# Kernel tuning notes

Hardware: AMD Instinct MI355X
Metric: run time of the kernel (lower is better)

## Reference

```python
import jax, jax.numpy as jnp
from jax import lax
import numpy as np

B, T, F, H, L = 256, 512, 16, 256, 2


def _lstm_layer(x, w_ih, w_hh, b_ih, b_hh):
    # x: [B, T, in]; w_ih: [4H, in]; w_hh: [4H, H]; biases: [4H]
    # PyTorch gate order: i, f, g, o
    x_proj = jnp.einsum('bti,gi->btg', x, w_ih) + b_ih + b_hh  # [B, T, 4H]
    h0 = jnp.zeros((x.shape[0], w_hh.shape[1]), x.dtype)
    c0 = h0

    def step(carry, xp):
        h, c = carry
        gates = xp + h @ w_hh.T  # [B, 4H]
        i, f, g, o = jnp.split(gates, 4, axis=-1)
        c = jax.nn.sigmoid(f) * c + jax.nn.sigmoid(i) * jnp.tanh(g)
        h = jax.nn.sigmoid(o) * jnp.tanh(c)
        return (h, c), h

    _, hs = lax.scan(step, (h0, c0), jnp.swapaxes(x_proj, 0, 1))  # [T, B, H]
    return jnp.swapaxes(hs, 0, 1)  # [B, T, H]


def setup_inputs() -> dict:
    key = jax.random.key(0)
    ks = jax.random.split(key, 16)
    x = jax.random.normal(ks[0], (B, T, F), dtype=jnp.float32)
    lengths = jax.random.randint(ks[1], (B,), 1, T + 1)  # in [1, T]
    s = 1.0 / np.sqrt(H)
    u = lambda k, shape: jax.random.uniform(k, shape, jnp.float32, -s, s)
    inp = {'x': x, 'lengths': lengths}
    in_dims = [F, H]
    for l in range(L):
        inp[f'w_ih{l}'] = u(ks[2 + 4 * l], (4 * H, in_dims[l]))
        inp[f'w_hh{l}'] = u(ks[3 + 4 * l], (4 * H, H))
        inp[f'b_ih{l}'] = u(ks[4 + 4 * l], (4 * H,))
        inp[f'b_hh{l}'] = u(ks[5 + 4 * l], (4 * H,))
    inp['fc_w'] = u(ks[10], (1, H))
    inp['fc_b'] = u(ks[11], (1,))
    return inp


def reference(x, lengths, w_ih0, w_hh0, b_ih0, b_hh0,
              w_ih1, w_hh1, b_ih1, b_hh1, fc_w, fc_b):
    # Packed LSTM: outputs at t >= length never influence last_outputs
    # (recurrence only flows forward in time), so running the dense
    # full-length LSTM and gathering at lengths-1 is mathematically identical.
    h = _lstm_layer(x, w_ih0, w_hh0, b_ih0, b_hh0)
    h = _lstm_layer(h, w_ih1, w_hh1, b_ih1, b_hh1)
    last = h[jnp.arange(h.shape[0]), lengths - 1]  # [B, H]
    return jax.nn.relu(last) @ fc_w.T + fc_b  # [B, 1]
```

## Files before the change

### kernel.cpp

```cpp
#include <hip/hip_runtime.h>
#include <hip/hip_fp16.h>


#define Tc 32
#define NCHUNK 16

#define OFF_IH0   0
#define OFF_B0    16384
#define OFF_B1    17408
#define OFF_C0S   18432
#define OFF_C1S   84480
#define OFF_H1S   150528
#define OFF_HLAST 216576
#define FP_END    282624
#define H_HH0  0
#define H_HH1  262144
#define H_IH1  524288
#define H_H0C  786432
#define H0SLOT 2113536
#define H_XP1  5013504
#define XPSLOT 8454144

#define SMEM_BYTES 149120
#define L0_WRES_OFF 50816
#define L1_WRES_OFF 17408

typedef _Float16 v2h __attribute__((ext_vector_type(2)));

__device__ __forceinline__ unsigned packh2(float a, float b) {
  __half2 h = __floats2half2_rn(a, b);
  return *(unsigned*)&h;
}
__device__ __forceinline__ float4 dot4(const float4 w, const v2h h, float4 acc) {
  const v2h* wg = (const v2h*)&w;
  acc.x = __builtin_amdgcn_fdot2(wg[0], h, acc.x, false);
  acc.y = __builtin_amdgcn_fdot2(wg[1], h, acc.y, false);
  acc.z = __builtin_amdgcn_fdot2(wg[2], h, acc.z, false);
  acc.w = __builtin_amdgcn_fdot2(wg[3], h, acc.w, false);
  return acc;
}
__device__ __forceinline__ float sigf(float x) {
  return __fdividef(1.f, 1.f + __expf(-x));
}
__device__ __forceinline__ float tanhf_fast(float x) {
  float ax = fabsf(x);
  float e = __expf(-2.f * ax);
  float t = __fdividef(1.f - e, 1.f + e);
  return copysignf(t, x);
}
__device__ __forceinline__ float h2f(unsigned short s) {
  __half h = __builtin_bit_cast(__half, s);
  return __half2float(h);
}
__device__ __forceinline__ float4 cvt4(ushort4 v) {
  float4 r;
  r.x = h2f(v.x); r.y = h2f(v.y); r.z = h2f(v.z); r.w = h2f(v.w);
  return r;
}
__device__ __forceinline__ v2h u2h(unsigned v) {
  return __builtin_bit_cast(v2h, v);
}
__device__ __forceinline__ void lds_barrier() {
  asm volatile("s_waitcnt lgkmcnt(0)" ::: "memory");
  __builtin_amdgcn_s_barrier();
  __builtin_amdgcn_sched_barrier(0);
}

__global__ __launch_bounds__(256) void prep_kernel(
    const float* __restrict__ w_ih0, const float* __restrict__ w_hh0,
    const float* __restrict__ b_ih0, const float* __restrict__ b_hh0,
    const float* __restrict__ w_ih1, const float* __restrict__ w_hh1,
    const float* __restrict__ b_ih1, const float* __restrict__ b_hh1,
    float* __restrict__ ws) {
  const int idx = blockIdx.x * blockDim.x + threadIdx.x;
  const int g = idx & 3, u = (idx >> 2) & 255, p = idx >> 10;
  const int j = g * 256 + u;
  unsigned* h16u = (unsigned*)(ws + FP_END);
  h16u[H_HH0 / 2 + idx] = packh2(w_hh0[j * 256 + 2 * p], w_hh0[j * 256 + 2 * p + 1]);
  h16u[H_HH1 / 2 + idx] = packh2(w_hh1[j * 256 + 2 * p], w_hh1[j * 256 + 2 * p + 1]);
  h16u[H_IH1 / 2 + idx] = packh2(w_ih1[j * 256 + 2 * p], w_ih1[j * 256 + 2 * p + 1]);
  if (idx < 8192) {
    ((unsigned*)(ws + OFF_IH0))[idx] =
        packh2(w_ih0[j * 16 + 2 * p], w_ih0[j * 16 + 2 * p + 1]);
  }
  if (idx < 1024) {
    ws[OFF_B0 + idx] = b_ih0[j] + b_hh0[j];
    ws[OFF_B1 + idx] = b_ih1[j] + b_hh1[j];
  }
}

__global__ __launch_bounds__(512)
__attribute__((amdgpu_waves_per_eu(2, 2)))
void fused_kernel(
    float* __restrict__ ws, const float* __restrict__ x,
    const int* __restrict__ lengths, int step) {
  extern __shared__ __align__(16) char smem_raw[];
  const int bid = blockIdx.x;
  const int tid = threadIdx.x;
  __half* h16 = (__half*)(ws + FP_END);
  unsigned short* h0cS = (unsigned short*)(h16 + H_H0C);
  unsigned short* xpS = (unsigned short*)(h16 + H_XP1);

  if (bid < 86) {
    if (step >= NCHUNK) return;
    const int kc = step;
    const int kh = tid >> 8, u = tid & 255;
    const int bg = bid * 3;
    unsigned short* hb = (unsigned short*)smem_raw;
    unsigned* xsp = (unsigned*)(smem_raw + 4096);
    float* scratch = (float*)(smem_raw + 4352);
    float4* wxl = (float4*)(smem_raw + 18048);
    float4* wres = (float4*)(smem_raw + L0_WRES_OFF);

    int len[3];
    #pragma unroll
    for (int b = 0; b < 3; ++b) len[b] = (bg + b < 256) ? lengths[bg + b] : 1;
    const int tmaxb = max(len[0], max(len[1], len[2]));
    if (kc * Tc >= tmaxb) return;
    const int tend = min(Tc, tmaxb - kc * Tc);
    const int slot = kc & 1, slotP = slot ^ 1;

    {
      const float4* gwx = (const float4*)(ws + OFF_IH0);
      #pragma unroll
      for (int e = 0; e < 4; ++e) wxl[tid + e * 512] = gwx[tid + e * 512];
    }
    {
      const float4* wgl = (const float4*)(h16 + H_HH0);
      #pragma unroll
      for (int e = 0; e < 12; ++e) {
        int i = tid + e * 512;
        int khh = (i >= 3072) ? 1 : 0;
        int r = i - khh * 3072;
        wres[i] = wgl[khh * 16384 + r];
      }
    }

    const float4* wq = (const float4*)(h16 + H_HH0) + (size_t)(kh * 64) * 256 + u;
    const float4* wrp = wres + kh * 3072 + u;
    const float4 bias = ((const float4*)(ws + OFF_B0))[u];

    float c[3] = {0.f, 0.f, 0.f};
    if (kh == 0) {
      #pragma unroll
      for (int b = 0; b < 3; ++b) {
        unsigned short hv = 0;
        if (kc > 0) {
          hv = h0cS[(size_t)slotP * H0SLOT + ((size_t)(bg + b) * 32 + 31) * 256 + u];
          c[b] = ws[OFF_C0S + (bg + b) * 256 + u];
        }
        hb[0 * 768 + b * 256 + u] = hv;
      }
    }
    if (tid < 24) {
      int b = tid >> 3, i = tid & 7;
      int bb = min(bg + b, 255);
      const float* xp = x + (size_t)bb * 8192 + (kc * Tc) * 16;
      xsp[0 * 24 + b * 8 + i] = packh2(xp[2 * i], xp[2 * i + 1]);
    }
    __syncthreads();

    float4 R[4][4];
    for (int tc = 0; tc < tend; ++tc) {
      const int cur = tc & 1, nxt = cur ^ 1;
      #pragma unroll
      for (int jp = 0; jp < 3; ++jp) {
        R[jp][0] = wq[((jp + 3) * 4 + 0) * 256];
        R[jp][1] = wq[((jp + 3) * 4 + 1) * 256];
        R[jp][2] = wq[((jp + 3) * 4 + 2) * 256];
        R[jp][3] = wq[((jp + 3) * 4 + 3) * 256];
      }
      float4 A0, A1, A2;
      if (kh == 0) { A0 = bias; A1 = bias; A2 = bias; }
      else { A0 = make_float4(0, 0, 0, 0); A1 = A0; A2 = A0; }

      #pragma unroll
      for (int p = 0; p < 4; ++p) {
        float4 w = wxl[(kh * 4 + p) * 256 + u];
        v2h x0 = u2h(xsp[cur * 24 + 0 * 8 + kh * 4 + p]);
        v2h x1 = u2h(xsp[cur * 24 + 1 * 8 + kh * 4 + p]);
        v2h x2 = u2h(xsp[cur * 24 + 2 * 8 + kh * 4 + p]);
        A0 = dot4(w, x0, A0);
        A1 = dot4(w, x1, A1);
        A2 = dot4(w, x2, A2);
      }

      const float4* h0r0 = (const float4*)(hb + cur * 768 + 0 * 256 + kh * 128);
      const float4* h0r1 = (const float4*)(hb + cur * 768 + 1 * 256 + kh * 128);
      const float4* h0r2 = (const float4*)(hb + cur * 768 + 2 * 256 + kh * 128);

      #pragma unroll
      for (int j = 0; j < 3; ++j) {
        float4 w0 = wrp[j * 1024 + 0 * 256];
        float4 w1 = wrp[j * 1024 + 1 * 256];
        float4 w2 = wrp[j * 1024 + 2 * 256];
        float4 w3 = wrp[j * 1024 + 3 * 256];
        float4 h40 = h0r0[j], h41 = h0r1[j], h42 = h0r2[j];
        const v2h* hp0 = (const v2h*)&h40;
        const v2h* hp1 = (const v2h*)&h41;
        const v2h* hp2 = (const v2h*)&h42;
        A0 = dot4(w0, hp0[0], A0); A0 = dot4(w1, hp0[1], A0);
        A0 = dot4(w2, hp0[2], A0); A0 = dot4(w3, hp0[3], A0);
        A1 = dot4(w0, hp1[0], A1); A1 = dot4(w1, hp1[1], A1);
        A1 = dot4(w2, hp1[2], A1); A1 = dot4(w3, hp1[3], A1);
        A2 = dot4(w0, hp2[0], A2); A2 = dot4(w1, hp2[1], A2);
        A2 = dot4(w2, hp2[2], A2); A2 = dot4(w3, hp2[3], A2);
      }
      #pragma unroll
      for (int j = 3; j < 16; ++j) {
        const int s = (j - 3) & 3;
        float4 w0 = R[s][0], w1 = R[s][1], w2 = R[s][2], w3 = R[s][3];
        if (j + 3 < 16) {
          R[j & 3][0] = wq[((j + 3) * 4 + 0) * 256];
          R[j & 3][1] = wq[((j + 3) * 4 + 1) * 256];
          R[j & 3][2] = wq[((j + 3) * 4 + 2) * 256];
          R[j & 3][3] = wq[((j + 3) * 4 + 3) * 256];
        }
        float4 h40 = h0r0[j], h41 = h0r1[j], h42 = h0r2[j];
        const v2h* hp0 = (const v2h*)&h40;
        const v2h* hp1 = (const v2h*)&h41;
        const v2h* hp2 = (const v2h*)&h42;
        A0 = dot4(w0, hp0[0], A0); A0 = dot4(w1, hp0[1], A0);
        A0 = dot4(w2, hp0[2], A0); A0 = dot4(w3, hp0[3], A0);
        A1 = dot4(w0, hp1[0], A1); A1 = dot4(w1, hp1[1], A1);
        A1 = dot4(w2, hp1[2], A1); A1 = dot4(w3, hp1[3], A1);
        A2 = dot4(w0, hp2[0], A2); A2 = dot4(w1, hp2[1], A2);
        A2 = dot4(w2, hp2[2], A2); A2 = dot4(w3, hp2[3], A2);
      }

      if (kh == 1) {
        #pragma unroll
        for (int g = 0; g < 4; ++g) {
          scratch[u * 13 + g] = ((const float*)&A0)[g];
          scratch[u * 13 + 4 + g] = ((const float*)&A1)[g];
          scratch[u * 13 + 8 + g] = ((const float*)&A2)[g];
        }
        if (tid < 256 + 24) {
          int bi = tid - 256, b = bi >> 3, i = bi & 7;
          int bb = min(bg + b, 255);
          int tn = min(kc * Tc + tc + 1, 511);
          const float* xp = x + (size_t)bb * 8192 + tn * 16;
          xsp[nxt * 24 + b * 8 + i] = packh2(xp[2 * i], xp[2 * i + 1]);
        }
      }
      lds_barrier();
      if (kh == 0) {
        float4 B0, B1, B2;
        #pragma unroll
        for (int g = 0; g < 4; ++g) {
          ((float*)&B0)[g] = scratch[u * 13 + g];
          ((float*)&B1)[g] = scratch[u * 13 + 4 + g];
          ((float*)&B2)[g] = scratch[u * 13 + 8 + g];
        }
        A0.x += B0.x; A0.y += B0.y; A0.z += B0.z; A0.w += B0.w;
        A1.x += B1.x; A1.y += B1.y; A1.z += B1.z; A1.w += B1.w;
        A2.x += B2.x; A2.y += B2.y; A2.z += B2.z; A2.w += B2.w;
        float4 A[3] = {A0, A1, A2};
        #pragma unroll
        for (int b = 0; b < 3; ++b) {
          float ig = sigf(A[b].x), fg = sigf(A[b].y);
          float gg = tanhf_fast(A[b].z), og = sigf(A[b].w);
          c[b] = fg * c[b] + ig * gg;
          float h = og * tanhf_fast(c[b]);
          unsigned short hu = __half_as_ushort(__float2half(h));
          hb[nxt * 768 + b * 256 + u] = hu;
          h0cS[(size_t)slot * H0SLOT + ((size_t)(bg + b) * 32 + tc) * 256 + u] = hu;
        }
      }
      lds_barrier();
    }
    if (kh == 0) {
      #pragma unroll
      for (int b = 0; b < 3; ++b) ws[OFF_C0S + (bg + b) * 256 + u] = c[b];
    }

  } else if (bid < 172) {
    if (step < 2 || step >= NCHUNK + 2) return;
    const int kc = step - 2;
    const int kh = tid >> 8, u = tid & 255;
    const int bg = (bid - 86) * 3;
    unsigned short* h1b = (unsigned short*)smem_raw;
    float* scratch = (float*)(smem_raw + 4096);
    float4* wres = (float4*)(smem_raw + L1_WRES_OFF);

    int len[3];
    #pragma unroll
    for (int b = 0; b < 3; ++b) len[b] = (bg + b < 256) ? lengths[bg + b] : 1;
    const int tmaxb = max(len[0], max(len[1], len[2]));
    if (kc * Tc >= tmaxb) return;
    const int tend = min(Tc, tmaxb - kc * Tc);
    const int slot = kc & 1;

    {
      const float4* wgl = (const float4*)(h16 + H_HH1);
      #pragma unroll
      for (int e = 0; e < 12; ++e) {
        int i = tid + e * 512;
        int khh = (i >= 3072) ? 1 : 0;
        int r = i - khh * 3072;
        wres[i] = wgl[khh * 16384 + r];
      }
    }
    const float4* wq = (const float4*)(h16 + H_HH1) + (size_t)(kh * 64) * 256 + u;
    const float4* wrp = wres + kh * 3072 + u;

    float c[3] = {0.f, 0.f, 0.f}, hout[3] = {0.f, 0.f, 0.f};
    if (kh == 0) {
      #pragma unroll
      for (int b = 0; b < 3; ++b) {
        float hv = 0.f;
        if (kc > 0) {
          hv = ws[OFF_H1S + (bg + b) * 256 + u];
          c[b] = ws[OFF_C1S + (bg + b) * 256 + u];
        }
        h1b[0 * 768 + b * 256 + u] = __half_as_ushort(__float2half(hv));
      }
    }
    const unsigned short* xb =
        xpS + (size_t)slot * XPSLOT + (size_t)bg * 32768 + u * 4;
    ushort4 xc0, xc1, xc2;
    if (kh == 0) {
      xc0 = *(const ushort4*)(xb);
      xc1 = *(const ushort4*)(xb + 32768);
      xc2 = *(const ushort4*)(xb + 65536);
    }
    __syncthreads();

    float4 R[4][4];
    for (int tc = 0; tc < tend; ++tc) {
      const int cur = tc & 1, nxt = cur ^ 1;
      #pragma unroll
      for (int jp = 0; jp < 3; ++jp) {
        R[jp][0] = wq[((jp + 3) * 4 + 0) * 256];
        R[jp][1] = wq[((jp + 3) * 4 + 1) * 256];
        R[jp][2] = wq[((jp + 3) * 4 + 2) * 256];
        R[jp][3] = wq[((jp + 3) * 4 + 3) * 256];
      }
      float4 A0, A1, A2;
      ushort4 xn0, xn1, xn2;
      if (kh == 0) {
        A0 = cvt4(xc0); A1 = cvt4(xc1); A2 = cvt4(xc2);
        if (tc + 1 < tend) {
          xn0 = *(const ushort4*)(xb + (tc + 1) * 1024);
          xn1 = *(const ushort4*)(xb + 32768 + (tc + 1) * 1024);
          xn2 = *(const ushort4*)(xb + 65536 + (tc + 1) * 1024);
        }
      } else { A0 = make_float4(0, 0, 0, 0); A1 = A0; A2 = A0; }

      const float4* r0 = (const float4*)(h1b + cur * 768 + 0 * 256 + kh * 128);
      const float4* r1 = (const float4*)(h1b + cur * 768 + 1 * 256 + kh * 128);
      const float4* r2 = (const float4*)(h1b + cur * 768 + 2 * 256 + kh * 128);

      #pragma unroll
      for (int j = 0; j < 3; ++j) {
        float4 w0 = wrp[j * 1024 + 0 * 256];
        float4 w1 = wrp[j * 1024 + 1 * 256];
        float4 w2 = wrp[j * 1024 + 2 * 256];
        float4 w3 = wrp[j * 1024 + 3 * 256];
        float4 h40 = r0[j], h41 = r1[j], h42 = r2[j];
        const v2h* hp0 = (const v2h*)&h40;
        const v2h* hp1 = (const v2h*)&h41;
        const v2h* hp2 = (const v2h*)&h42;
        A0 = dot4(w0, hp0[0], A0); A0 = dot4(w1, hp0[1], A0);
        A0 = dot4(w2, hp0[2], A0); A0 = dot4(w3, hp0[3], A0);
        A1 = dot4(w0, hp1[0], A1); A1 = dot4(w1, hp1[1], A1);
        A1 = dot4(w2, hp1[2], A1); A1 = dot4(w3, hp1[3], A1);
        A2 = dot4(w0, hp2[0], A2); A2 = dot4(w1, hp2[1], A2);
        A2 = dot4(w2, hp2[2], A2); A2 = dot4(w3, hp2[3], A2);
      }
      #pragma unroll
      for (int j = 3; j < 16; ++j) {
        const int s = (j - 3) & 3;
        float4 w0 = R[s][0], w1 = R[s][1], w2 = R[s][2], w3 = R[s][3];
        if (j + 3 < 16) {
          R[j & 3][0] = wq[((j + 3) * 4 + 0) * 256];
          R[j & 3][1] = wq[((j + 3) * 4 + 1) * 256];
          R[j & 3][2] = wq[((j + 3) * 4 + 2) * 256];
          R[j & 3][3] = wq[((j + 3) * 4 + 3) * 256];
        }
        float4 h40 = r0[j], h41 = r1[j], h42 = r2[j];
        const v2h* hp0 = (const v2h*)&h40;
        const v2h* hp1 = (const v2h*)&h41;
        const v2h* hp2 = (const v2h*)&h42;
        A0 = dot4(w0, hp0[0], A0); A0 = dot4(w1, hp0[1], A0);
        A0 = dot4(w2, hp0[2], A0); A0 = dot4(w3, hp0[3], A0);
        A1 = dot4(w0, hp1[0], A1); A1 = dot4(w1, hp1[1], A1);
        A1 = dot4(w2, hp1[2], A1); A1 = dot4(w3, hp1[3], A1);
        A2 = dot4(w0, hp2[0], A2); A2 = dot4(w1, hp2[1], A2);
        A2 = dot4(w2, hp2[2], A2); A2 = dot4(w3, hp2[3], A2);
      }

      if (kh == 1) {
        #pragma unroll
        for (int g = 0; g < 4; ++g) {
          scratch[u * 13 + g] = ((const float*)&A0)[g];
          scratch[u * 13 + 4 + g] = ((const float*)&A1)[g];
          scratch[u * 13 + 8 + g] = ((const float*)&A2)[g];
        }
      }
      lds_barrier();
      if (kh == 0) {
        float4 B0, B1, B2;
        #pragma unroll
        for (int g = 0; g < 4; ++g) {
          ((float*)&B0)[g] = scratch[u * 13 + g];
          ((float*)&B1)[g] = scratch[u * 13 + 4 + g];
          ((float*)&B2)[g] = scratch[u * 13 + 8 + g];
        }
        A0.x += B0.x; A0.y += B0.y; A0.z += B0.z; A0.w += B0.w;
        A1.x += B1.x; A1.y += B1.y; A1.z += B1.z; A1.w += B1.w;
        A2.x += B2.x; A2.y += B2.y; A2.z += B2.z; A2.w += B2.w;
        float4 A[3] = {A0, A1, A2};
        const int t = kc * Tc + tc;
        #pragma unroll
        for (int b = 0; b < 3; ++b) {
          float ig = sigf(A[b].x), fg = sigf(A[b].y);
          float gg = tanhf_fast(A[b].z), og = sigf(A[b].w);
          c[b] = fg * c[b] + ig * gg;
          float h = og * tanhf_fast(c[b]);
          hout[b] = h;
          h1b[nxt * 768 + b * 256 + u] = __half_as_ushort(__float2half(h));
          if (t == len[b] - 1) ws[OFF_HLAST + (bg + b) * 256 + u] = h;
        }
        xc0 = xn0; xc1 = xn1; xc2 = xn2;
      }
      lds_barrier();
    }
    if (kh == 0) {
      #pragma unroll
      for (int b = 0; b < 3; ++b) {
        ws[OFF_C1S + (bg + b) * 256 + u] = c[b];
        ws[OFF_H1S + (bg + b) * 256 + u] = hout[b];
      }
    }

  } else {
    if (step < 1 || step >= NCHUNK + 1) return;
    if (bid >= 236) return;
    const int kc = step - 1;
    const int gid = bid - 172;
    const int b0g = gid * 4;
    const int rt = tid & 63, wv = tid >> 6;
    __half2* hc2 = (__half2*)smem_raw;

    int lmax = 0;
    #pragma unroll
    for (int i = 0; i < 4; ++i) lmax = max(lmax, lengths[b0g + i]);
    if (kc * Tc >= lmax) return;
    const int slot = kc & 1;

    {
      const unsigned short* src =
          h0cS + (size_t)slot * H0SLOT + (size_t)b0g * 8192;
      const int cl = tid & 127, pg = tid >> 7;
      #pragma unroll
      for (int pp = 0; pp < 32; pp += 4) {
        const int p0 = pg * 32 + pp;
        uint4 v = *(const uint4*)(src + (size_t)cl * 256 + p0 * 2);
        unsigned* d = (unsigned*)hc2;
        d[(p0 + 0) * 128 + cl] = v.x;
        d[(p0 + 1) * 128 + cl] = v.y;
        d[(p0 + 2) * 128 + cl] = v.z;
        d[(p0 + 3) * 128 + cl] = v.w;
      }
    }
    __syncthreads();

    const __half* Wb = h16 + H_IH1;
    unsigned short* xdst = xpS + (size_t)slot * XPSLOT;
    #pragma unroll 1
    for (int rp = 0; rp < 2; ++rp) {
      #pragma unroll 1
      for (int cp = 0; cp < 2; ++cp) {
        const int uA = rp * 128 + rt, uB = uA + 64;
        const int c0 = cp * 64 + wv * 8;
        const float4 bA = ((const float4*)(ws + OFF_B1))[uA];
        const float4 bB = ((const float4*)(ws + OFF_B1))[uB];
        float accA[4][8], accB[4][8];
        #pragma unroll
        for (int g = 0; g < 4; ++g)
          #pragma unroll
          for (int cc = 0; cc < 8; ++cc) {
            accA[g][cc] = ((const float*)&bA)[g];
            accB[g][cc] = ((const float*)&bB)[g];
          }
        #pragma unroll 2
        for (int p = 0; p < 128; ++p) {
          float4 wA = *(const float4*)(Wb + (size_t)p * 2048 + uA * 8);
          float4 wB = *(const float4*)(Wb + (size_t)p * 2048 + uB * 8);
          float4 h0v = *(const float4*)(hc2 + p * 128 + c0);
          float4 h1v = *(const float4*)(hc2 + p * 128 + c0 + 4);
          const v2h* ga = (const v2h*)&wA;
          const v2h* gb = (const v2h*)&wB;
          const v2h* hv = (const v2h*)&h0v;
          const v2h* hw = (const v2h*)&h1v;
          #pragma unroll
          for (int g = 0; g < 4; ++g) {
            #pragma unroll
            for (int cc = 0; cc < 4; ++cc) {
              accA[g][cc] = __builtin_amdgcn_fdot2(ga[g], hv[cc], accA[g][cc], false);
              accA[g][cc + 4] = __builtin_amdgcn_fdot2(ga[g], hw[cc], accA[g][cc + 4], false);
              accB[g][cc] = __builtin_amdgcn_fdot2(gb[g], hv[cc], accB[g][cc], false);
              accB[g][cc + 4] = __builtin_amdgcn_fdot2(gb[g], hw[cc], accB[g][cc + 4], false);
            }
          }
        }
        #pragma unroll
        for (int cc = 0; cc < 8; ++cc) {
          const int col = c0 + cc;
          const size_t cb = ((size_t)(b0g + (col >> 5)) * 32 + (col & 31)) * 1024;
          ushort4 oA, oB;
          oA.x = __half_as_ushort(__float2half(accA[0][cc]));
          oA.y = __half_as_ushort(__float2half(accA[1][cc]));
          oA.z = __half_as_ushort(__float2half(accA[2][cc]));
          oA.w = __half_as_ushort(__float2half(accA[3][cc]));
          oB.x = __half_as_ushort(__float2half(accB[0][cc]));
          oB.y = __half_as_ushort(__float2half(accB[1][cc]));
          oB.z = __half_as_ushort(__float2half(accB[2][cc]));
          oB.w = __half_as_ushort(__float2half(accB[3][cc]));
          *(ushort4*)(xdst + cb + uA * 4) = oA;
          *(ushort4*)(xdst + cb + uB * 4) = oB;
        }
      }
    }
  }
}

__global__ __launch_bounds__(256) void fc_kernel(
    const float* __restrict__ ws, const float* __restrict__ fc_w,
    const float* __restrict__ fc_b, float* __restrict__ out) {
  __shared__ float red[256];
  const int tid = threadIdx.x;
  const int b = blockIdx.x;
  red[tid] = fmaxf(ws[OFF_HLAST + b * 256 + tid], 0.f) * fc_w[tid];
  __syncthreads();
  #pragma unroll
  for (int s = 128; s > 0; s >>= 1) {
    if (tid < s) red[tid] += red[tid + s];
    __syncthreads();
  }
  if (tid == 0) out[b] = red[0] + fc_b[0];
}

extern "C" void kernel_launch(void* const* d_in, const int* in_sizes, int n_in,
                              void* d_out, int out_size, void* d_ws, size_t ws_size,
                              hipStream_t stream) {
  const float* x     = (const float*)d_in[0];
  const int*   lens  = (const int*)d_in[1];
  const float* w_ih0 = (const float*)d_in[2];
  const float* w_hh0 = (const float*)d_in[3];
  const float* b_ih0 = (const float*)d_in[4];
  const float* b_hh0 = (const float*)d_in[5];
  const float* w_ih1 = (const float*)d_in[6];
  const float* w_hh1 = (const float*)d_in[7];
  const float* b_ih1 = (const float*)d_in[8];
  const float* b_hh1 = (const float*)d_in[9];
  const float* fc_w  = (const float*)d_in[10];
  const float* fc_b  = (const float*)d_in[11];
  float* out = (float*)d_out;
  float* ws  = (float*)d_ws;

  hipLaunchKernelGGL(prep_kernel, dim3(512), dim3(256), 0, stream,
                     w_ih0, w_hh0, b_ih0, b_hh0, w_ih1, w_hh1, b_ih1, b_hh1, ws);
  hipFuncSetAttribute(reinterpret_cast<const void*>(fused_kernel),
                      hipFuncAttributeMaxDynamicSharedMemorySize, SMEM_BYTES);
  for (int k = 0; k < NCHUNK + 2; ++k) {
    hipLaunchKernelGGL(fused_kernel, dim3(236), dim3(512), SMEM_BYTES, stream,
                       ws, x, lens, k);
  }
  hipLaunchKernelGGL(fc_kernel, dim3(256), dim3(256), 0, stream,
                     ws, fc_w, fc_b, out);
}
```

Baseline: 2.934 ms.

## Replace per-chunk kernel launches with one cooperative persistent kernel using grid sync

```diff
diff --git a/kernel.cpp b/kernel.cpp
--- a/kernel.cpp
+++ b/kernel.cpp
@@ -1,5 +1,6 @@
 #include <hip/hip_runtime.h>
 #include <hip/hip_fp16.h>
+#include <hip/hip_cooperative_groups.h>
 
 
 #define Tc 32
@@ -91,9 +92,9 @@
 
 __global__ __launch_bounds__(512)
 __attribute__((amdgpu_waves_per_eu(2, 2)))
-void fused_kernel(
-    float* __restrict__ ws, const float* __restrict__ x,
-    const int* __restrict__ lengths, int step) {
+void fused_all(float* __restrict__ ws, const float* __restrict__ x,
+               const int* __restrict__ lengths) {
+  cooperative_groups::grid_group grid = cooperative_groups::this_grid();
   extern __shared__ __align__(16) char smem_raw[];
   const int bid = blockIdx.x;
   const int tid = threadIdx.x;
@@ -102,8 +103,6 @@
   unsigned short* xpS = (unsigned short*)(h16 + H_XP1);
 
   if (bid < 86) {
-    if (step >= NCHUNK) return;
-    const int kc = step;
     const int kh = tid >> 8, u = tid & 255;
     const int bg = bid * 3;
     unsigned short* hb = (unsigned short*)smem_raw;
@@ -112,20 +111,10 @@
     float4* wxl = (float4*)(smem_raw + 18048);
     float4* wres = (float4*)(smem_raw + L0_WRES_OFF);
 
-    int len[3];
-    #pragma unroll
-    for (int b = 0; b < 3; ++b) len[b] = (bg + b < 256) ? lengths[bg + b] : 1;
-    const int tmaxb = max(len[0], max(len[1], len[2]));
-    if (kc * Tc >= tmaxb) return;
-    const int tend = min(Tc, tmaxb - kc * Tc);
-    const int slot = kc & 1, slotP = slot ^ 1;
-
     {
       const float4* gwx = (const float4*)(ws + OFF_IH0);
       #pragma unroll
       for (int e = 0; e < 4; ++e) wxl[tid + e * 512] = gwx[tid + e * 512];
-    }
-    {
       const float4* wgl = (const float4*)(h16 + H_HH0);
       #pragma unroll
       for (int e = 0; e < 12; ++e) {
@@ -135,161 +124,163 @@
         wres[i] = wgl[khh * 16384 + r];
       }
     }
-
     const float4* wq = (const float4*)(h16 + H_HH0) + (size_t)(kh * 64) * 256 + u;
     const float4* wrp = wres + kh * 3072 + u;
     const float4 bias = ((const float4*)(ws + OFF_B0))[u];
-
-    float c[3] = {0.f, 0.f, 0.f};
-    if (kh == 0) {
-      #pragma unroll
-      for (int b = 0; b < 3; ++b) {
-        unsigned short hv = 0;
-        if (kc > 0) {
-          hv = h0cS[(size_t)slotP * H0SLOT + ((size_t)(bg + b) * 32 + 31) * 256 + u];
-          c[b] = ws[OFF_C0S + (bg + b) * 256 + u];
-        }
-        hb[0 * 768 + b * 256 + u] = hv;
+    int len[3];
+    #pragma unroll
+    for (int b = 0; b < 3; ++b) len[b] = (bg + b < 256) ? lengths[bg + b] : 1;
+    const int tmaxb = max(len[0], max(len[1], len[2]));
+
+    for (int step = 0; step < NCHUNK + 2; ++step) {
+      if (step < NCHUNK && step * Tc < tmaxb) {
+        const int kc = step;
+        const int tend = min(Tc, tmaxb - kc * Tc);
+        const int slot = kc & 1, slotP = slot ^ 1;
+
+        float c[3] = {0.f, 0.f, 0.f};
+        if (kh == 0) {
+          #pragma unroll
+          for (int b = 0; b < 3; ++b) {
+            unsigned short hv = 0;
+            if (kc > 0) {
+              hv = h0cS[(size_t)slotP * H0SLOT + ((size_t)(bg + b) * 32 + 31) * 256 + u];
+              c[b] = ws[OFF_C0S + (bg + b) * 256 + u];
+            }
+            hb[0 * 768 + b * 256 + u] = hv;
+          }
+        }
+        if (tid < 24) {
+          int b = tid >> 3, i = tid & 7;
+          int bb = min(bg + b, 255);
+          const float* xp = x + (size_t)bb * 8192 + (kc * Tc) * 16;
+          xsp[0 * 24 + b * 8 + i] = packh2(xp[2 * i], xp[2 * i + 1]);
+        }
+        __syncthreads();
+
+        float4 R[4][4];
+        for (int tc = 0; tc < tend; ++tc) {
+          const int cur = tc & 1, nxt = cur ^ 1;
+          #pragma unroll
+          for (int jp = 0; jp < 3; ++jp) {
+            R[jp][0] = wq[((jp + 3) * 4 + 0) * 256];
+            R[jp][1] = wq[((jp + 3) * 4 + 1) * 256];
+            R[jp][2] = wq[((jp + 3) * 4 + 2) * 256];
+            R[jp][3] = wq[((jp + 3) * 4 + 3) * 256];
+          }
+          float4 A0, A1, A2;
+          if (kh == 0) { A0 = bias; A1 = bias; A2 = bias; }
+          else { A0 = make_float4(0, 0, 0, 0); A1 = A0; A2 = A0; }
+
+          #pragma unroll
+          for (int p = 0; p < 4; ++p) {
+            float4 w = wxl[(kh * 4 + p) * 256 + u];
+            v2h x0 = u2h(xsp[cur * 24 + 0 * 8 + kh * 4 + p]);
+            v2h x1 = u2h(xsp[cur * 24 + 1 * 8 + kh * 4 + p]);
+            v2h x2 = u2h(xsp[cur * 24 + 2 * 8 + kh * 4 + p]);
+            A0 = dot4(w, x0, A0);
+            A1 = dot4(w, x1, A1);
+            A2 = dot4(w, x2, A2);
+          }
+
+          const float4* h0r0 = (const float4*)(hb + cur * 768 + 0 * 256 + kh * 128);
+          const float4* h0r1 = (const float4*)(hb + cur * 768 + 1 * 256 + kh * 128);
+          const float4* h0r2 = (const float4*)(hb + cur * 768 + 2 * 256 + kh * 128);
+
+          #pragma unroll
+          for (int j = 0; j < 3; ++j) {
+            float4 w0 = wrp[j * 1024 + 0 * 256];
+            float4 w1 = wrp[j * 1024 + 1 * 256];
+            float4 w2 = wrp[j * 1024 + 2 * 256];
+            float4 w3 = wrp[j * 1024 + 3 * 256];
+            float4 h40 = h0r0[j], h41 = h0r1[j], h42 = h0r2[j];
+            const v2h* hp0 = (const v2h*)&h40;
+            const v2h* hp1 = (const v2h*)&h41;
+            const v2h* hp2 = (const v2h*)&h42;
+            A0 = dot4(w0, hp0[0], A0); A0 = dot4(w1, hp0[1], A0);
+            A0 = dot4(w2, hp0[2], A0); A0 = dot4(w3, hp0[3], A0);
+            A1 = dot4(w0, hp1[0], A1); A1 = dot4(w1, hp1[1], A1);
+            A1 = dot4(w2, hp1[2], A1); A1 = dot4(w3, hp1[3], A1);
+            A2 = dot4(w0, hp2[0], A2); A2 = dot4(w1, hp2[1], A2);
+            A2 = dot4(w2, hp2[2], A2); A2 = dot4(w3, hp2[3], A2);
+          }
+          #pragma unroll
+          for (int j = 3; j < 16; ++j) {
+            const int s = (j - 3) & 3;
+            float4 w0 = R[s][0], w1 = R[s][1], w2 = R[s][2], w3 = R[s][3];
+            if (j + 3 < 16) {
+              R[j & 3][0] = wq[((j + 3) * 4 + 0) * 256];
+              R[j & 3][1] = wq[((j + 3) * 4 + 1) * 256];
+              R[j & 3][2] = wq[((j + 3) * 4 + 2) * 256];
+              R[j & 3][3] = wq[((j + 3) * 4 + 3) * 256];
+            }
+            float4 h40 = h0r0[j], h41 = h0r1[j], h42 = h0r2[j];
+            const v2h* hp0 = (const v2h*)&h40;
+            const v2h* hp1 = (const v2h*)&h41;
+            const v2h* hp2 = (const v2h*)&h42;
+            A0 = dot4(w0, hp0[0], A0); A0 = dot4(w1, hp0[1], A0);
+            A0 = dot4(w2, hp0[2], A0); A0 = dot4(w3, hp0[3], A0);
+            A1 = dot4(w0, hp1[0], A1); A1 = dot4(w1, hp1[1], A1);
+            A1 = dot4(w2, hp1[2], A1); A1 = dot4(w3, hp1[3], A1);
+            A2 = dot4(w0, hp2[0], A2); A2 = dot4(w1, hp2[1], A2);
+            A2 = dot4(w2, hp2[2], A2); A2 = dot4(w3, hp2[3], A2);
+          }
+
+          if (kh == 1) {
+            #pragma unroll
+            for (int g = 0; g < 4; ++g) {
+              scratch[u * 13 + g] = ((const float*)&A0)[g];
+              scratch[u * 13 + 4 + g] = ((const float*)&A1)[g];
+              scratch[u * 13 + 8 + g] = ((const float*)&A2)[g];
+            }
+            if (tid < 256 + 24) {
+              int bi = tid - 256, b = bi >> 3, i = bi & 7;
+              int bb = min(bg + b, 255);
+              int tn = min(kc * Tc + tc + 1, 511);
+              const float* xp = x + (size_t)bb * 8192 + tn * 16;
+              xsp[nxt * 24 + b * 8 + i] = packh2(xp[2 * i], xp[2 * i + 1]);
+            }
+          }
+          lds_barrier();
+          if (kh == 0) {
+            float4 B0, B1, B2;
+            #pragma unroll
+            for (int g = 0; g < 4; ++g) {
+              ((float*)&B0)[g] = scratch[u * 13 + g];
+              ((float*)&B1)[g] = scratch[u * 13 + 4 + g];
+              ((float*)&B2)[g] = scratch[u * 13 + 8 + g];
+            }
+            A0.x += B0.x; A0.y += B0.y; A0.z += B0.z; A0.w += B0.w;
+            A1.x += B1.x; A1.y += B1.y; A1.z += B1.z; A1.w += B1.w;
+            A2.x += B2.x; A2.y += B2.y; A2.z += B2.z; A2.w += B2.w;
+            float4 A[3] = {A0, A1, A2};
+            #pragma unroll
+            for (int b = 0; b < 3; ++b) {
+              float ig = sigf(A[b].x), fg = sigf(A[b].y);
+              float gg = tanhf_fast(A[b].z), og = sigf(A[b].w);
+              c[b] = fg * c[b] + ig * gg;
+              float h = og * tanhf_fast(c[b]);
+              unsigned short hu = __half_as_ushort(__float2half(h));
+              hb[nxt * 768 + b * 256 + u] = hu;
+              h0cS[(size_t)slot * H0SLOT + ((size_t)(bg + b) * 32 + tc) * 256 + u] = hu;
+            }
+          }
+          lds_barrier();
+        }
+        if (kh == 0) {
+          #pragma unroll
+          for (int b = 0; b < 3; ++b) ws[OFF_C0S + (bg + b) * 256 + u] = c[b];
+        }
       }
+      grid.sync();
     }
-    if (tid < 24) {
-      int b = tid >> 3, i = tid & 7;
-      int bb = min(bg + b, 255);
-      const float* xp = x + (size_t)bb * 8192 + (kc * Tc) * 16;
-      xsp[0 * 24 + b * 8 + i] = packh2(xp[2 * i], xp[2 * i + 1]);
-    }
-    __syncthreads();
-
-    float4 R[4][4];
-    for (int tc = 0; tc < tend; ++tc) {
-      const int cur = tc & 1, nxt = cur ^ 1;
-      #pragma unroll
-      for (int jp = 0; jp < 3; ++jp) {
-        R[jp][0] = wq[((jp + 3) * 4 + 0) * 256];
-        R[jp][1] = wq[((jp + 3) * 4 + 1) * 256];
-        R[jp][2] = wq[((jp + 3) * 4 + 2) * 256];
-        R[jp][3] = wq[((jp + 3) * 4 + 3) * 256];
-      }
-      float4 A0, A1, A2;
-      if (kh == 0) { A0 = bias; A1 = bias; A2 = bias; }
-      else { A0 = make_float4(0, 0, 0, 0); A1 = A0; A2 = A0; }
-
-      #pragma unroll
-      for (int p = 0; p < 4; ++p) {
-        float4 w = wxl[(kh * 4 + p) * 256 + u];
-        v2h x0 = u2h(xsp[cur * 24 + 0 * 8 + kh * 4 + p]);
-        v2h x1 = u2h(xsp[cur * 24 + 1 * 8 + kh * 4 + p]);
-        v2h x2 = u2h(xsp[cur * 24 + 2 * 8 + kh * 4 + p]);
-        A0 = dot4(w, x0, A0);
-        A1 = dot4(w, x1, A1);
-        A2 = dot4(w, x2, A2);
-      }
-
-      const float4* h0r0 = (const float4*)(hb + cur * 768 + 0 * 256 + kh * 128);
-      const float4* h0r1 = (const float4*)(hb + cur * 768 + 1 * 256 + kh * 128);
-      const float4* h0r2 = (const float4*)(hb + cur * 768 + 2 * 256 + kh * 128);
-
-      #pragma unroll
-      for (int j = 0; j < 3; ++j) {
-        float4 w0 = wrp[j * 1024 + 0 * 256];
-        float4 w1 = wrp[j * 1024 + 1 * 256];
-        float4 w2 = wrp[j * 1024 + 2 * 256];
-        float4 w3 = wrp[j * 1024 + 3 * 256];
-        float4 h40 = h0r0[j], h41 = h0r1[j], h42 = h0r2[j];
-        const v2h* hp0 = (const v2h*)&h40;
-        const v2h* hp1 = (const v2h*)&h41;
-        const v2h* hp2 = (const v2h*)&h42;
-        A0 = dot4(w0, hp0[0], A0); A0 = dot4(w1, hp0[1], A0);
-        A0 = dot4(w2, hp0[2], A0); A0 = dot4(w3, hp0[3], A0);
-        A1 = dot4(w0, hp1[0], A1); A1 = dot4(w1, hp1[1], A1);
-        A1 = dot4(w2, hp1[2], A1); A1 = dot4(w3, hp1[3], A1);
-        A2 = dot4(w0, hp2[0], A2); A2 = dot4(w1, hp2[1], A2);
-        A2 = dot4(w2, hp2[2], A2); A2 = dot4(w3, hp2[3], A2);
-      }
-      #pragma unroll
-      for (int j = 3; j < 16; ++j) {
-        const int s = (j - 3) & 3;
-        float4 w0 = R[s][0], w1 = R[s][1], w2 = R[s][2], w3 = R[s][3];
-        if (j + 3 < 16) {
-          R[j & 3][0] = wq[((j + 3) * 4 + 0) * 256];
-          R[j & 3][1] = wq[((j + 3) * 4 + 1) * 256];
-          R[j & 3][2] = wq[((j + 3) * 4 + 2) * 256];
-          R[j & 3][3] = wq[((j + 3) * 4 + 3) * 256];
-        }
-        float4 h40 = h0r0[j], h41 = h0r1[j], h42 = h0r2[j];
-        const v2h* hp0 = (const v2h*)&h40;
-        const v2h* hp1 = (const v2h*)&h41;
-        const v2h* hp2 = (const v2h*)&h42;
-        A0 = dot4(w0, hp0[0], A0); A0 = dot4(w1, hp0[1], A0);
-        A0 = dot4(w2, hp0[2], A0); A0 = dot4(w3, hp0[3], A0);
-        A1 = dot4(w0, hp1[0], A1); A1 = dot4(w1, hp1[1], A1);
-        A1 = dot4(w2, hp1[2], A1); A1 = dot4(w3, hp1[3], A1);
-        A2 = dot4(w0, hp2[0], A2); A2 = dot4(w1, hp2[1], A2);
-        A2 = dot4(w2, hp2[2], A2); A2 = dot4(w3, hp2[3], A2);
-      }
-
-      if (kh == 1) {
-        #pragma unroll
-        for (int g = 0; g < 4; ++g) {
-          scratch[u * 13 + g] = ((const float*)&A0)[g];
-          scratch[u * 13 + 4 + g] = ((const float*)&A1)[g];
-          scratch[u * 13 + 8 + g] = ((const float*)&A2)[g];
-        }
-        if (tid < 256 + 24) {
-          int bi = tid - 256, b = bi >> 3, i = bi & 7;
-          int bb = min(bg + b, 255);
-          int tn = min(kc * Tc + tc + 1, 511);
-          const float* xp = x + (size_t)bb * 8192 + tn * 16;
-          xsp[nxt * 24 + b * 8 + i] = packh2(xp[2 * i], xp[2 * i + 1]);
-        }
-      }
-      lds_barrier();
-      if (kh == 0) {
-        float4 B0, B1, B2;
-        #pragma unroll
-        for (int g = 0; g < 4; ++g) {
-          ((float*)&B0)[g] = scratch[u * 13 + g];
-          ((float*)&B1)[g] = scratch[u * 13 + 4 + g];
-          ((float*)&B2)[g] = scratch[u * 13 + 8 + g];
-        }
-        A0.x += B0.x; A0.y += B0.y; A0.z += B0.z; A0.w += B0.w;
-        A1.x += B1.x; A1.y += B1.y; A1.z += B1.z; A1.w += B1.w;
-        A2.x += B2.x; A2.y += B2.y; A2.z += B2.z; A2.w += B2.w;
-        float4 A[3] = {A0, A1, A2};
-        #pragma unroll
-        for (int b = 0; b < 3; ++b) {
-          float ig = sigf(A[b].x), fg = sigf(A[b].y);
-          float gg = tanhf_fast(A[b].z), og = sigf(A[b].w);
-          c[b] = fg * c[b] + ig * gg;
-          float h = og * tanhf_fast(c[b]);
-          unsigned short hu = __half_as_ushort(__float2half(h));
-          hb[nxt * 768 + b * 256 + u] = hu;
-          h0cS[(size_t)slot * H0SLOT + ((size_t)(bg + b) * 32 + tc) * 256 + u] = hu;
-        }
-      }
-      lds_barrier();
-    }
-    if (kh == 0) {
-      #pragma unroll
-      for (int b = 0; b < 3; ++b) ws[OFF_C0S + (bg + b) * 256 + u] = c[b];
-    }
 
   } else if (bid < 172) {
-    if (step < 2 || step >= NCHUNK + 2) return;
-    const int kc = step - 2;
     const int kh = tid >> 8, u = tid & 255;
     const int bg = (bid - 86) * 3;
     unsigned short* h1b = (unsigned short*)smem_raw;
     float* scratch = (float*)(smem_raw + 4096);
     float4* wres = (float4*)(smem_raw + L1_WRES_OFF);
-
-    int len[3];
-    #pragma unroll
-    for (int b = 0; b < 3; ++b) len[b] = (bg + b < 256) ? lengths[bg + b] : 1;
-    const int tmaxb = max(len[0], max(len[1], len[2]));
-    if (kc * Tc >= tmaxb) return;
-    const int tend = min(Tc, tmaxb - kc * Tc);
-    const int slot = kc & 1;
 
     {
       const float4* wgl = (const float4*)(h16 + H_HH1);
@@ -303,225 +294,241 @@
     }
     const float4* wq = (const float4*)(h16 + H_HH1) + (size_t)(kh * 64) * 256 + u;
     const float4* wrp = wres + kh * 3072 + u;
-
-    float c[3] = {0.f, 0.f, 0.f}, hout[3] = {0.f, 0.f, 0.f};
-    if (kh == 0) {
-      #pragma unroll
-      for (int b = 0; b < 3; ++b) {
-        float hv = 0.f;
-        if (kc > 0) {
-          hv = ws[OFF_H1S + (bg + b) * 256 + u];
-          c[b] = ws[OFF_C1S + (bg + b) * 256 + u];
-        }
-        h1b[0 * 768 + b * 256 + u] = __half_as_ushort(__float2half(hv));
+    int len[3];
+    #pragma unroll
+    for (int b = 0; b < 3; ++b) len[b] = (bg + b < 256) ? lengths[bg + b] : 1;
+    const int tmaxb = max(len[0], max(len[1], len[2]));
+
+    for (int step = 0; step < NCHUNK + 2; ++step) {
+      if (step >= 2 && (step - 2) * Tc < tmaxb) {
+        const int kc = step - 2;
+        const int tend = min(Tc, tmaxb - kc * Tc);
+        const int slot = kc & 1;
+
+        float c[3] = {0.f, 0.f, 0.f}, hout[3] = {0.f, 0.f, 0.f};
+        if (kh == 0) {
+          #pragma unroll
+          for (int b = 0; b < 3; ++b) {
+            float hv = 0.f;
+            if (kc > 0) {
+              hv = ws[OFF_H1S + (bg + b) * 256 + u];
+              c[b] = ws[OFF_C1S + (bg + b) * 256 + u];
+            }
+            h1b[0 * 768 + b * 256 + u] = __half_as_ushort(__float2half(hv));
+          }
+        }
+        const unsigned short* xb =
+            xpS + (size_t)slot * XPSLOT + (size_t)bg * 32768 + u * 4;
+        ushort4 xc0, xc1, xc2;
+        if (kh == 0) {
+          xc0 = *(const ushort4*)(xb);
+          xc1 = *(const ushort4*)(xb + 32768);
+          xc2 = *(const ushort4*)(xb + 65536);
+        }
+        __syncthreads();
+
+        float4 R[4][4];
+        for (int tc = 0; tc < tend; ++tc) {
+          const int cur = tc & 1, nxt = cur ^ 1;
+          #pragma unroll
+          for (int jp = 0; jp < 3; ++jp) {
+            R[jp][0] = wq[((jp + 3) * 4 + 0) * 256];
+            R[jp][1] = wq[((jp + 3) * 4 + 1) * 256];
+            R[jp][2] = wq[((jp + 3) * 4 + 2) * 256];
+            R[jp][3] = wq[((jp + 3) * 4 + 3) * 256];
+          }
+          float4 A0, A1, A2;
+          ushort4 xn0, xn1, xn2;
+          if (kh == 0) {
+            A0 = cvt4(xc0); A1 = cvt4(xc1); A2 = cvt4(xc2);
+            if (tc + 1 < tend) {
+              xn0 = *(const ushort4*)(xb + (tc + 1) * 1024);
+              xn1 = *(const ushort4*)(xb + 32768 + (tc + 1) * 1024);
+              xn2 = *(const ushort4*)(xb + 65536 + (tc + 1) * 1024);
+            }
+          } else { A0 = make_float4(0, 0, 0, 0); A1 = A0; A2 = A0; }
+
+          const float4* r0 = (const float4*)(h1b + cur * 768 + 0 * 256 + kh * 128);
+          const float4* r1 = (const float4*)(h1b + cur * 768 + 1 * 256 + kh * 128);
+          const float4* r2 = (const float4*)(h1b + cur * 768 + 2 * 256 + kh * 128);
+
+          #pragma unroll
+          for (int j = 0; j < 3; ++j) {
+            float4 w0 = wrp[j * 1024 + 0 * 256];
+            float4 w1 = wrp[j * 1024 + 1 * 256];
+            float4 w2 = wrp[j * 1024 + 2 * 256];
+            float4 w3 = wrp[j * 1024 + 3 * 256];
+            float4 h40 = r0[j], h41 = r1[j], h42 = r2[j];
+            const v2h* hp0 = (const v2h*)&h40;
+            const v2h* hp1 = (const v2h*)&h41;
+            const v2h* hp2 = (const v2h*)&h42;
+            A0 = dot4(w0, hp0[0], A0); A0 = dot4(w1, hp0[1], A0);
+            A0 = dot4(w2, hp0[2], A0); A0 = dot4(w3, hp0[3], A0);
+            A1 = dot4(w0, hp1[0], A1); A1 = dot4(w1, hp1[1], A1);
+            A1 = dot4(w2, hp1[2], A1); A1 = dot4(w3, hp1[3], A1);
+            A2 = dot4(w0, hp2[0], A2); A2 = dot4(w1, hp2[1], A2);
+            A2 = dot4(w2, hp2[2], A2); A2 = dot4(w3, hp2[3], A2);
+          }
+          #pragma unroll
+          for (int j = 3; j < 16; ++j) {
+            const int s = (j - 3) & 3;
+            float4 w0 = R[s][0], w1 = R[s][1], w2 = R[s][2], w3 = R[s][3];
+            if (j + 3 < 16) {
+              R[j & 3][0] = wq[((j + 3) * 4 + 0) * 256];
+              R[j & 3][1] = wq[((j + 3) * 4 + 1) * 256];
+              R[j & 3][2] = wq[((j + 3) * 4 + 2) * 256];
+              R[j & 3][3] = wq[((j + 3) * 4 + 3) * 256];
+            }
+            float4 h40 = r0[j], h41 = r1[j], h42 = r2[j];
+            const v2h* hp0 = (const v2h*)&h40;
+            const v2h* hp1 = (const v2h*)&h41;
+            const v2h* hp2 = (const v2h*)&h42;
+            A0 = dot4(w0, hp0[0], A0); A0 = dot4(w1, hp0[1], A0);
+            A0 = dot4(w2, hp0[2], A0); A0 = dot4(w3, hp0[3], A0);
+            A1 = dot4(w0, hp1[0], A1); A1 = dot4(w1, hp1[1], A1);
+            A1 = dot4(w2, hp1[2], A1); A1 = dot4(w3, hp1[3], A1);
+            A2 = dot4(w0, hp2[0], A2); A2 = dot4(w1, hp2[1], A2);
+            A2 = dot4(w2, hp2[2], A2); A2 = dot4(w3, hp2[3], A2);
+          }
+
+          if (kh == 1) {
+            #pragma unroll
+            for (int g = 0; g < 4; ++g) {
+              scratch[u * 13 + g] = ((const float*)&A0)[g];
+              scratch[u * 13 + 4 + g] = ((const float*)&A1)[g];
+              scratch[u * 13 + 8 + g] = ((const float*)&A2)[g];
+            }
+          }
+          lds_barrier();
+          if (kh == 0) {
+            float4 B0, B1, B2;
+            #pragma unroll
+            for (int g = 0; g < 4; ++g) {
+              ((float*)&B0)[g] = scratch[u * 13 + g];
+              ((float*)&B1)[g] = scratch[u * 13 + 4 + g];
+              ((float*)&B2)[g] = scratch[u * 13 + 8 + g];
+            }
+            A0.x += B0.x; A0.y += B0.y; A0.z += B0.z; A0.w += B0.w;
+            A1.x += B1.x; A1.y += B1.y; A1.z += B1.z; A1.w += B1.w;
+            A2.x += B2.x; A2.y += B2.y; A2.z += B2.z; A2.w += B2.w;
+            float4 A[3] = {A0, A1, A2};
+            const int t = kc * Tc + tc;
+            #pragma unroll
+            for (int b = 0; b < 3; ++b) {
+              float ig = sigf(A[b].x), fg = sigf(A[b].y);
+              float gg = tanhf_fast(A[b].z), og = sigf(A[b].w);
+              c[b] = fg * c[b] + ig * gg;
+              float h = og * tanhf_fast(c[b]);
+              hout[b] = h;
+              h1b[nxt * 768 + b * 256 + u] = __half_as_ushort(__float2half(h));
+              if (t == len[b] - 1) ws[OFF_HLAST + (bg + b) * 256 + u] = h;
+            }
+            xc0 = xn0; xc1 = xn1; xc2 = xn2;
+          }
+          lds_barrier();
+        }
+        if (kh == 0) {
+          #pragma unroll
+          for (int b = 0; b < 3; ++b) {
+            ws[OFF_C1S + (bg + b) * 256 + u] = c[b];
+            ws[OFF_H1S + (bg + b) * 256 + u] = hout[b];
+          }
+        }
       }
+      grid.sync();
     }
-    const unsigned short* xb =
-        xpS + (size_t)slot * XPSLOT + (size_t)bg * 32768 + u * 4;
-    ushort4 xc0, xc1, xc2;
-    if (kh == 0) {
-      xc0 = *(const ushort4*)(xb);
-      xc1 = *(const ushort4*)(xb + 32768);
-      xc2 = *(const ushort4*)(xb + 65536);
-    }
-    __syncthreads();
-
-    float4 R[4][4];
-    for (int tc = 0; tc < tend; ++tc) {
-      const int cur = tc & 1, nxt = cur ^ 1;
-      #pragma unroll
-      for (int jp = 0; jp < 3; ++jp) {
-        R[jp][0] = wq[((jp + 3) * 4 + 0) * 256];
-        R[jp][1] = wq[((jp + 3) * 4 + 1) * 256];
-        R[jp][2] = wq[((jp + 3) * 4 + 2) * 256];
-        R[jp][3] = wq[((jp + 3) * 4 + 3) * 256];
-      }
-      float4 A0, A1, A2;
-      ushort4 xn0, xn1, xn2;
-      if (kh == 0) {
-        A0 = cvt4(xc0); A1 = cvt4(xc1); A2 = cvt4(xc2);
-        if (tc + 1 < tend) {
-          xn0 = *(const ushort4*)(xb + (tc + 1) * 1024);
-          xn1 = *(const ushort4*)(xb + 32768 + (tc + 1) * 1024);
-          xn2 = *(const ushort4*)(xb + 65536 + (tc + 1) * 1024);
-        }
-      } else { A0 = make_float4(0, 0, 0, 0); A1 = A0; A2 = A0; }
-
-      const float4* r0 = (const float4*)(h1b + cur * 768 + 0 * 256 + kh * 128);
-      const float4* r1 = (const float4*)(h1b + cur * 768 + 1 * 256 + kh * 128);
-      const float4* r2 = (const float4*)(h1b + cur * 768 + 2 * 256 + kh * 128);
-
-      #pragma unroll
-      for (int j = 0; j < 3; ++j) {
-        float4 w0 = wrp[j * 1024 + 0 * 256];
-        float4 w1 = wrp[j * 1024 + 1 * 256];
-        float4 w2 = wrp[j * 1024 + 2 * 256];
-        float4 w3 = wrp[j * 1024 + 3 * 256];
-        float4 h40 = r0[j], h41 = r1[j], h42 = r2[j];
-        const v2h* hp0 = (const v2h*)&h40;
-        const v2h* hp1 = (const v2h*)&h41;
-        const v2h* hp2 = (const v2h*)&h42;
-        A0 = dot4(w0, hp0[0], A0); A0 = dot4(w1, hp0[1], A0);
-        A0 = dot4(w2, hp0[2], A0); A0 = dot4(w3, hp0[3], A0);
-        A1 = dot4(w0, hp1[0], A1); A1 = dot4(w1, hp1[1], A1);
-        A1 = dot4(w2, hp1[2], A1); A1 = dot4(w3, hp1[3], A1);
-        A2 = dot4(w0, hp2[0], A2); A2 = dot4(w1, hp2[1], A2);
-        A2 = dot4(w2, hp2[2], A2); A2 = dot4(w3, hp2[3], A2);
-      }
-      #pragma unroll
-      for (int j = 3; j < 16; ++j) {
-        const int s = (j - 3) & 3;
-        float4 w0 = R[s][0], w1 = R[s][1], w2 = R[s][2], w3 = R[s][3];
-        if (j + 3 < 16) {
-          R[j & 3][0] = wq[((j + 3) * 4 + 0) * 256];
-          R[j & 3][1] = wq[((j + 3) * 4 + 1) * 256];
-          R[j & 3][2] = wq[((j + 3) * 4 + 2) * 256];
-          R[j & 3][3] = wq[((j + 3) * 4 + 3) * 256];
-        }
-        float4 h40 = r0[j], h41 = r1[j], h42 = r2[j];
-        const v2h* hp0 = (const v2h*)&h40;
-        const v2h* hp1 = (const v2h*)&h41;
-        const v2h* hp2 = (const v2h*)&h42;
-        A0 = dot4(w0, hp0[0], A0); A0 = dot4(w1, hp0[1], A0);
-        A0 = dot4(w2, hp0[2], A0); A0 = dot4(w3, hp0[3], A0);
-        A1 = dot4(w0, hp1[0], A1); A1 = dot4(w1, hp1[1], A1);
-        A1 = dot4(w2, hp1[2], A1); A1 = dot4(w3, hp1[3], A1);
-        A2 = dot4(w0, hp2[0], A2); A2 = dot4(w1, hp2[1], A2);
-        A2 = dot4(w2, hp2[2], A2); A2 = dot4(w3, hp2[3], A2);
-      }
-
-      if (kh == 1) {
-        #pragma unroll
-        for (int g = 0; g < 4; ++g) {
-          scratch[u * 13 + g] = ((const float*)&A0)[g];
-          scratch[u * 13 + 4 + g] = ((const float*)&A1)[g];
-          scratch[u * 13 + 8 + g] = ((const float*)&A2)[g];
-        }
-      }
-      lds_barrier();
-      if (kh == 0) {
-        float4 B0, B1, B2;
-        #pragma unroll
-        for (int g = 0; g < 4; ++g) {
-          ((float*)&B0)[g] = scratch[u * 13 + g];
-          ((float*)&B1)[g] = scratch[u * 13 + 4 + g];
-          ((float*)&B2)[g] = scratch[u * 13 + 8 + g];
-        }
-        A0.x += B0.x; A0.y += B0.y; A0.z += B0.z; A0.w += B0.w;
-        A1.x += B1.x; A1.y += B1.y; A1.z += B1.z; A1.w += B1.w;
-        A2.x += B2.x; A2.y += B2.y; A2.z += B2.z; A2.w += B2.w;
-        float4 A[3] = {A0, A1, A2};
-        const int t = kc * Tc + tc;
-        #pragma unroll
-        for (int b = 0; b < 3; ++b) {
-          float ig = sigf(A[b].x), fg = sigf(A[b].y);
-          float gg = tanhf_fast(A[b].z), og = sigf(A[b].w);
-          c[b] = fg * c[b] + ig * gg;
-          float h = og * tanhf_fast(c[b]);
-          hout[b] = h;
-          h1b[nxt * 768 + b * 256 + u] = __half_as_ushort(__float2half(h));
-          if (t == len[b] - 1) ws[OFF_HLAST + (bg + b) * 256 + u] = h;
-        }
-        xc0 = xn0; xc1 = xn1; xc2 = xn2;
-      }
-      lds_barrier();
-    }
-    if (kh == 0) {
-      #pragma unroll
-      for (int b = 0; b < 3; ++b) {
-        ws[OFF_C1S + (bg + b) * 256 + u] = c[b];
-        ws[OFF_H1S + (bg + b) * 256 + u] = hout[b];
-      }
-    }
 
   } else {
-    if (step < 1 || step >= NCHUNK + 1) return;
-    if (bid >= 236) return;
-    const int kc = step - 1;
     const int gid = bid - 172;
     const int b0g = gid * 4;
     const int rt = tid & 63, wv = tid >> 6;
     __half2* hc2 = (__half2*)smem_raw;
-
     int lmax = 0;
     #pragma unroll
     for (int i = 0; i < 4; ++i) lmax = max(lmax, lengths[b0g + i]);
-    if (kc * Tc >= lmax) return;
-    const int slot = kc & 1;
-
-    {
-      const unsigned short* src =
-          h0cS + (size_t)slot * H0SLOT + (size_t)b0g * 8192;
-      const int cl = tid & 127, pg = tid >> 7;
-      #pragma unroll
-      for (int pp = 0; pp < 32; pp += 4) {
-        const int p0 = pg * 32 + pp;
-        uint4 v = *(const uint4*)(src + (size_t)cl * 256 + p0 * 2);
-        unsigned* d = (unsigned*)hc2;
-        d[(p0 + 0) * 128 + cl] = v.x;
-        d[(p0 + 1) * 128 + cl] = v.y;
-        d[(p0 + 2) * 128 + cl] = v.z;
-        d[(p0 + 3) * 128 + cl] = v.w;
+
+    for (int step = 0; step < NCHUNK + 2; ++step) {
+      if (step >= 1 && step < NCHUNK + 1 && (step - 1) * Tc < lmax) {
+        const int kc = step - 1;
+        const int slot = kc & 1;
+        __syncthreads();
+
+        {
+          const unsigned short* src =
+              h0cS + (size_t)slot * H0SLOT + (size_t)b0g * 8192;
+          const int cl = tid & 127, pg = tid >> 7;
+          #pragma unroll
+          for (int pp = 0; pp < 32; pp += 4) {
+            const int p0 = pg * 32 + pp;
+            uint4 v = *(const uint4*)(src + (size_t)cl * 256 + p0 * 2);
+            unsigned* d = (unsigned*)hc2;
+            d[(p0 + 0) * 128 + cl] = v.x;
+            d[(p0 + 1) * 128 + cl] = v.y;
+            d[(p0 + 2) * 128 + cl] = v.z;
+            d[(p0 + 3) * 128 + cl] = v.w;
+          }
+        }
+        __syncthreads();
+
+        const __half* Wb = h16 + H_IH1;
+        unsigned short* xdst = xpS + (size_t)slot * XPSLOT;
+        #pragma unroll 1
+        for (int rp = 0; rp < 2; ++rp) {
+          #pragma unroll 1
+          for (int cp = 0; cp < 2; ++cp) {
+            const int uA = rp * 128 + rt, uB = uA + 64;
+            const int c0 = cp * 64 + wv * 8;
+            const float4 bA = ((const float4*)(ws + OFF_B1))[uA];
+            const float4 bB = ((const float4*)(ws + OFF_B1))[uB];
+            float accA[4][8], accB[4][8];
+            #pragma unroll
+            for (int g = 0; g < 4; ++g)
+              #pragma unroll
+              for (int cc = 0; cc < 8; ++cc) {
+                accA[g][cc] = ((const float*)&bA)[g];
+                accB[g][cc] = ((const float*)&bB)[g];
+              }
+            #pragma unroll 2
+            for (int p = 0; p < 128; ++p) {
+              float4 wA = *(const float4*)(Wb + (size_t)p * 2048 + uA * 8);
+              float4 wB = *(const float4*)(Wb + (size_t)p * 2048 + uB * 8);
+              float4 h0v = *(const float4*)(hc2 + p * 128 + c0);
+              float4 h1v = *(const float4*)(hc2 + p * 128 + c0 + 4);
+              const v2h* ga = (const v2h*)&wA;
+              const v2h* gb = (const v2h*)&wB;
+              const v2h* hv = (const v2h*)&h0v;
+              const v2h* hw = (const v2h*)&h1v;
+              #pragma unroll
+              for (int g = 0; g < 4; ++g) {
+                #pragma unroll
+                for (int cc = 0; cc < 4; ++cc) {
+                  accA[g][cc] = __builtin_amdgcn_fdot2(ga[g], hv[cc], accA[g][cc], false);
+                  accA[g][cc + 4] = __builtin_amdgcn_fdot2(ga[g], hw[cc], accA[g][cc + 4], false);
+                  accB[g][cc] = __builtin_amdgcn_fdot2(gb[g], hv[cc], accB[g][cc], false);
+                  accB[g][cc + 4] = __builtin_amdgcn_fdot2(gb[g], hw[cc], accB[g][cc + 4], false);
+                }
+              }
+            }
+            #pragma unroll
+            for (int cc = 0; cc < 8; ++cc) {
+              const int col = c0 + cc;
+              const size_t cb = ((size_t)(b0g + (col >> 5)) * 32 + (col & 31)) * 1024;
+              ushort4 oA, oB;
+              oA.x = __half_as_ushort(__float2half(accA[0][cc]));
+              oA.y = __half_as_ushort(__float2half(accA[1][cc]));
+              oA.z = __half_as_ushort(__float2half(accA[2][cc]));
+              oA.w = __half_as_ushort(__float2half(accA[3][cc]));
+              oB.x = __half_as_ushort(__float2half(accB[0][cc]));
+              oB.y = __half_as_ushort(__float2half(accB[1][cc]));
+              oB.z = __half_as_ushort(__float2half(accB[2][cc]));
+              oB.w = __half_as_ushort(__float2half(accB[3][cc]));
+              *(ushort4*)(xdst + cb + uA * 4) = oA;
+              *(ushort4*)(xdst + cb + uB * 4) = oB;
+            }
+          }
+        }
       }
-    }
-    __syncthreads();
-
-    const __half* Wb = h16 + H_IH1;
-    unsigned short* xdst = xpS + (size_t)slot * XPSLOT;
-    #pragma unroll 1
-    for (int rp = 0; rp < 2; ++rp) {
-      #pragma unroll 1
-      for (int cp = 0; cp < 2; ++cp) {
-        const int uA = rp * 128 + rt, uB = uA + 64;
-        const int c0 = cp * 64 + wv * 8;
-        const float4 bA = ((const float4*)(ws + OFF_B1))[uA];
-        const float4 bB = ((const float4*)(ws + OFF_B1))[uB];
-        float accA[4][8], accB[4][8];
-        #pragma unroll
-        for (int g = 0; g < 4; ++g)
-          #pragma unroll
-          for (int cc = 0; cc < 8; ++cc) {
-            accA[g][cc] = ((const float*)&bA)[g];
-            accB[g][cc] = ((const float*)&bB)[g];
-          }
-        #pragma unroll 2
-        for (int p = 0; p < 128; ++p) {
-          float4 wA = *(const float4*)(Wb + (size_t)p * 2048 + uA * 8);
-          float4 wB = *(const float4*)(Wb + (size_t)p * 2048 + uB * 8);
-          float4 h0v = *(const float4*)(hc2 + p * 128 + c0);
-          float4 h1v = *(const float4*)(hc2 + p * 128 + c0 + 4);
-          const v2h* ga = (const v2h*)&wA;
-          const v2h* gb = (const v2h*)&wB;
-          const v2h* hv = (const v2h*)&h0v;
-          const v2h* hw = (const v2h*)&h1v;
-          #pragma unroll
-          for (int g = 0; g < 4; ++g) {
-            #pragma unroll
-            for (int cc = 0; cc < 4; ++cc) {
-              accA[g][cc] = __builtin_amdgcn_fdot2(ga[g], hv[cc], accA[g][cc], false);
-              accA[g][cc + 4] = __builtin_amdgcn_fdot2(ga[g], hw[cc], accA[g][cc + 4], false);
-              accB[g][cc] = __builtin_amdgcn_fdot2(gb[g], hv[cc], accB[g][cc], false);
-              accB[g][cc + 4] = __builtin_amdgcn_fdot2(gb[g], hw[cc], accB[g][cc + 4], false);
-            }
-          }
-        }
-        #pragma unroll
-        for (int cc = 0; cc < 8; ++cc) {
-          const int col = c0 + cc;
-          const size_t cb = ((size_t)(b0g + (col >> 5)) * 32 + (col & 31)) * 1024;
-          ushort4 oA, oB;
-          oA.x = __half_as_ushort(__float2half(accA[0][cc]));
-          oA.y = __half_as_ushort(__float2half(accA[1][cc]));
-          oA.z = __half_as_ushort(__float2half(accA[2][cc]));
-          oA.w = __half_as_ushort(__float2half(accA[3][cc]));
-          oB.x = __half_as_ushort(__float2half(accB[0][cc]));
-          oB.y = __half_as_ushort(__float2half(accB[1][cc]));
-          oB.z = __half_as_ushort(__float2half(accB[2][cc]));
-          oB.w = __half_as_ushort(__float2half(accB[3][cc]));
-          *(ushort4*)(xdst + cb + uA * 4) = oA;
-          *(ushort4*)(xdst + cb + uB * 4) = oB;
-        }
-      }
+      grid.sync();
     }
   }
 }
@@ -562,12 +569,11 @@
 
   hipLaunchKernelGGL(prep_kernel, dim3(512), dim3(256), 0, stream,
                      w_ih0, w_hh0, b_ih0, b_hh0, w_ih1, w_hh1, b_ih1, b_hh1, ws);
-  hipFuncSetAttribute(reinterpret_cast<const void*>(fused_kernel),
+  hipFuncSetAttribute(reinterpret_cast<const void*>(fused_all),
                       hipFuncAttributeMaxDynamicSharedMemorySize, SMEM_BYTES);
-  for (int k = 0; k < NCHUNK + 2; ++k) {
-    hipLaunchKernelGGL(fused_kernel, dim3(236), dim3(512), SMEM_BYTES, stream,
-                       ws, x, lens, k);
-  }
+  void* args[] = {(void*)&ws, (void*)&x, (void*)&lens};
+  hipLaunchCooperativeKernel(reinterpret_cast<void*>(fused_all),
+                             dim3(236), dim3(512), args, SMEM_BYTES, stream);
   hipLaunchKernelGGL(fc_kernel, dim3(256), dim3(256), 0, stream,
                      ws, fc_w, fc_b, out);
 }
```

Result: slower. 3.377 ms (+15.1%).
